# Performance work log

Measured on AMD Instinct MI355X. Metric: run time of the kernel, lower is better.

The kernel has to match this reference:

```python
import jax, jax.numpy as jnp
import numpy as np

N, M, D = 100000, 5000, 2

def setup_inputs() -> dict:
    key = jax.random.key(0)
    k1, k2, k3 = jax.random.split(key, 3)
    euclidean_data = jax.random.normal(k1, (N, D), dtype=jnp.float32)
    maze_points = jax.random.normal(k2, (M, D), dtype=jnp.float32)
    ts_proj = jax.random.uniform(k3, (M,), dtype=jnp.float32)
    return {"euclidean_data": euclidean_data, "maze_points": maze_points, "ts_proj": ts_proj}

def reference(euclidean_data, maze_points, ts_proj):
    # squared distance matrix [N, M], reduced via argmin (1-NN)
    diff = euclidean_data[:, None, :] - maze_points[None, :, :]   # [N, M, D]
    dist2 = jnp.sum(jnp.square(diff), axis=-1)                    # [N, M]
    best = jnp.argmin(dist2, axis=1)                              # [N]
    projected_pos = maze_points[best]                             # [N, D]
    linear_pos = ts_proj[best]                                    # [N]
    return (projected_pos, linear_pos)
```

## Files before the change

kernel.cpp:

```cpp
#include <hip/hip_runtime.h>

#define N_Q  100000
#define N_M  5000
#define G    64
#define NC   (G * G)
#define RMAX 4
#define CS_OFF_B   64
#define SORT_OFF_B (CS_OFF_B + 16400)
#define OVF_OFF_B  (SORT_OFF_B + N_M * 16)
#define WS_NEED    (OVF_OFF_B + N_Q * 4)

__global__ __launch_bounds__(1024) void build_grid(
    const float* __restrict__ maze, const float* __restrict__ ts,
    float* __restrict__ ws)
{
    __shared__ float red[1024];
    __shared__ int   part[1024];
    __shared__ int   cnt[NC];
    const int t = threadIdx.x;
    if (t == 0) ((int*)ws)[8] = 0;

    float mnx = 1e30f, mxx = -1e30f, mny = 1e30f, mxy = -1e30f;
    for (int i = t; i < N_M; i += 1024) {
        const float x = maze[2 * i], y = maze[2 * i + 1];
        mnx = fminf(mnx, x); mxx = fmaxf(mxx, x);
        mny = fminf(mny, y); mxy = fmaxf(mxy, y);
    }
    auto reduce = [&](float v, bool domin) -> float {
        red[t] = v; __syncthreads();
        for (int s = 512; s > 0; s >>= 1) {
            if (t < s) {
                const float o = red[t + s];
                red[t] = domin ? fminf(red[t], o) : fmaxf(red[t], o);
            }
            __syncthreads();
        }
        const float r = red[0]; __syncthreads(); return r;
    };
    mnx = reduce(mnx, true);  mxx = reduce(mxx, false);
    mny = reduce(mny, true);  mxy = reduce(mxy, false);

    float cwx = (mxx - mnx) * (1.0f / G) * (1.0f + 1e-5f);
    float cwy = (mxy - mny) * (1.0f / G) * (1.0f + 1e-5f);
    if (!(cwx > 0.0f)) cwx = 1.0f;
    if (!(cwy > 0.0f)) cwy = 1.0f;
    const float ivx = 1.0f / cwx, ivy = 1.0f / cwy;
    if (t == 0) {
        ws[0] = mnx; ws[1] = mny; ws[2] = cwx;
        ws[3] = cwy; ws[4] = ivx; ws[5] = ivy;
    }

    for (int i = t; i < NC; i += 1024) cnt[i] = 0;
    __syncthreads();
    for (int i = t; i < N_M; i += 1024) {
        const float x = maze[2 * i], y = maze[2 * i + 1];
        const int cx = min(G - 1, max(0, (int)((x - mnx) * ivx)));
        const int cy = min(G - 1, max(0, (int)((y - mny) * ivy)));
        atomicAdd(&cnt[cy * G + cx], 1);
    }
    __syncthreads();

    int* cs = (int*)((char*)ws + CS_OFF_B);
    const int base = t * 4;
    int loc[4], sum = 0;
    #pragma unroll
    for (int j = 0; j < 4; ++j) { loc[j] = sum; sum += cnt[base + j]; }
    part[t] = sum; __syncthreads();
    for (int s = 1; s < 1024; s <<= 1) {
        const int v = (t >= s) ? part[t - s] : 0;
        __syncthreads();
        part[t] += v;
        __syncthreads();
    }
    const int excl = part[t] - sum;
    #pragma unroll
    for (int j = 0; j < 4; ++j) cs[base + j] = excl + loc[j];
    if (t == 0) cs[NC] = N_M;
    __syncthreads();
    #pragma unroll
    for (int j = 0; j < 4; ++j) cnt[base + j] = excl + loc[j];
    __syncthreads();

    float4* sorted = (float4*)((char*)ws + SORT_OFF_B);
    for (int i = t; i < N_M; i += 1024) {
        const float x = maze[2 * i], y = maze[2 * i + 1];
        const int cx = min(G - 1, max(0, (int)((x - mnx) * ivx)));
        const int cy = min(G - 1, max(0, (int)((y - mny) * ivy)));
        const int pos = atomicAdd(&cnt[cy * G + cx], 1);
        float4 e; e.x = x; e.y = y; e.z = ts[i]; e.w = __int_as_float(i);
        sorted[pos] = e;
    }
}

__global__ __launch_bounds__(256) void grid_query(
    const float* __restrict__ q, const float* __restrict__ maze,
    const float* __restrict__ ts, float* __restrict__ ws,
    float* __restrict__ out)
{
    const int qi = blockIdx.x * 256 + threadIdx.x;
    if (qi >= N_Q) return;

    const float mnx = ws[0], mny = ws[1], cwx = ws[2];
    const float cwy = ws[3], ivx = ws[4], ivy = ws[5];
    const int*    cs     = (const int*)((const char*)ws + CS_OFF_B);
    const float4* sorted = (const float4*)((const char*)ws + SORT_OFF_B);

    const float2 Q = ((const float2*)q)[qi];
    const float qx = Q.x, qy = Q.y;
    const int cx = min(G - 1, max(0, (int)((qx - mnx) * ivx)));
    const int cy = min(G - 1, max(0, (int)((qy - mny) * ivy)));

    float bd2 = 3.4e38f;
    int bidx = 0x7fffffff;

    auto cand = [&](const float4 c) {
        const float dx = __fsub_rn(qx, c.x);
        const float dy = __fsub_rn(qy, c.y);
        const float d2 = __fadd_rn(__fmul_rn(dx, dx), __fmul_rn(dy, dy));
        const int idx = __float_as_int(c.w);
        if (d2 < bd2 || (d2 == bd2 && idx < bidx)) { bd2 = d2; bidx = idx; }
    };
    auto scan8 = [&](int s, int e) {
        for (int p = s; p < e; p += 8) {
            const float4 c0 = sorted[p];
            const float4 c1 = sorted[p + 1 < e ? p + 1 : p];
            const float4 c2 = sorted[p + 2 < e ? p + 2 : p];
            const float4 c3 = sorted[p + 3 < e ? p + 3 : p];
            const float4 c4 = sorted[p + 4 < e ? p + 4 : p];
            const float4 c5 = sorted[p + 5 < e ? p + 5 : p];
            const float4 c6 = sorted[p + 6 < e ? p + 6 : p];
            const float4 c7 = sorted[p + 7 < e ? p + 7 : p];
            cand(c0); cand(c1); cand(c2); cand(c3);
            cand(c4); cand(c5); cand(c6); cand(c7);
        }
    };
    auto scan4 = [&](int s, int e) {
        for (int p = s; p < e; p += 4) {
            const float4 c0 = sorted[p];
            const float4 c1 = sorted[p + 1 < e ? p + 1 : p];
            const float4 c2 = sorted[p + 2 < e ? p + 2 : p];
            const float4 c3 = sorted[p + 3 < e ? p + 3 : p];
            cand(c0); cand(c1); cand(c2); cand(c3);
        }
    };
    auto bound_ok = [&](int r) -> bool {
        const float Xlo = mnx + (float)(cx - r) * cwx;
        const float Xhi = mnx + (float)(cx + r + 1) * cwx;
        const float Ylo = mny + (float)(cy - r) * cwy;
        const float Yhi = mny + (float)(cy + r + 1) * cwy;
        float lb = fminf(fminf(qx - Xlo, Xhi - qx), fminf(qy - Ylo, Yhi - qy));
        lb = lb * 0.9999f - 1e-6f;
        return (lb > 0.0f) && (lb * lb > bd2);
    };

    {
        const int x0 = max(0, cx - 1), x1 = min(G - 1, cx + 1);
        const int rA = max(0, cy - 1) * G, rB = cy * G, rC = min(G - 1, cy + 1) * G;
        const int sA = cs[rA + x0], eA = cs[rA + x1 + 1];
        const int sB = cs[rB + x0], eB = cs[rB + x1 + 1];
        const int sC = cs[rC + x0], eC = cs[rC + x1 + 1];
        scan8(sA, eA); scan8(sB, eB); scan8(sC, eC);
    }
    bool resolved = bound_ok(1);

    for (int r = 2; r <= RMAX && __any(!resolved); ++r) {
        if (!resolved) {
            const int X0 = max(0, cx - r), X1 = min(G - 1, cx + r);
            if (cy - r >= 0)     { const int rb = (cy - r) * G; scan8(cs[rb + X0], cs[rb + X1 + 1]); }
            if (cy + r <= G - 1) { const int rb = (cy + r) * G; scan8(cs[rb + X0], cs[rb + X1 + 1]); }
            const int Y0 = max(0, cy - r + 1), Y1 = min(G - 1, cy + r - 1);
            if (cx - r >= 0)     for (int y = Y0; y <= Y1; ++y) { const int c0 = y * G + cx - r; scan4(cs[c0], cs[c0 + 1]); }
            if (cx + r <= G - 1) for (int y = Y0; y <= Y1; ++y) { const int c0 = y * G + cx + r; scan4(cs[c0], cs[c0 + 1]); }
            resolved = bound_ok(r);
        }
    }

    if (resolved) {
        out[2 * qi]       = maze[2 * bidx];
        out[2 * qi + 1]   = maze[2 * bidx + 1];
        out[2 * N_Q + qi] = ts[bidx];
    } else {
        int* ovfc = (int*)ws + 8;
        const int pos = atomicAdd(ovfc, 1);
        ((int*)((char*)ws + OVF_OFF_B))[pos] = qi;
    }
}

__global__ __launch_bounds__(256) void brute_overflow(
    const float* __restrict__ q, const float* __restrict__ maze,
    const float* __restrict__ ts, const float* __restrict__ ws,
    float* __restrict__ out)
{
    const int cnt = ((const int*)ws)[8];
    const int* ovl = (const int*)((const char*)ws + OVF_OFF_B);
    const int wave  = (blockIdx.x * 256 + threadIdx.x) >> 6;
    const int lane  = threadIdx.x & 63;
    const int nwave = gridDim.x * 4;

    for (int w = wave; w < cnt; w += nwave) {
        const int qi = ovl[w];
        const float qx = q[2 * qi], qy = q[2 * qi + 1];
        float bd2 = 3.4e38f; int bidx = 0x7fffffff;
        for (int p = lane; p < N_M; p += 64) {
            const float2 c = ((const float2*)maze)[p];
            const float dx = __fsub_rn(qx, c.x);
            const float dy = __fsub_rn(qy, c.y);
            const float d2 = __fadd_rn(__fmul_rn(dx, dx), __fmul_rn(dy, dy));
            if (d2 < bd2 || (d2 == bd2 && p < bidx)) { bd2 = d2; bidx = p; }
        }
        #pragma unroll
        for (int s = 1; s < 64; s <<= 1) {
            const float ob = __shfl_xor(bd2, s);
            const int   oi = __shfl_xor(bidx, s);
            if (ob < bd2 || (ob == bd2 && oi < bidx)) { bd2 = ob; bidx = oi; }
        }
        if (lane == 0) {
            out[2 * qi]       = maze[2 * bidx];
            out[2 * qi + 1]   = maze[2 * bidx + 1];
            out[2 * N_Q + qi] = ts[bidx];
        }
    }
}

#define CW   4
#define CHK  1264
#define NPAD (CW * CHK)

typedef float v2f __attribute__((ext_vector_type(2)));
typedef float v8f __attribute__((ext_vector_type(8)));

__global__ void setup_soa(const float* __restrict__ maze, float* __restrict__ ws) {
    const int i = blockIdx.x * 256 + threadIdx.x;
    if (i >= NPAD) return;
    const int c = i / CHK, k = i - c * CHK;
    float x = 1e30f, y = 1e30f;
    const int g = c * 1250 + k;
    if (k < 1250) { x = -maze[2 * g]; y = -maze[2 * g + 1]; }
    ws[i] = x;
    ws[NPAD + i] = y;
}

#define LDX0(D) asm volatile("s_load_dwordx8 %0, %1, 0x0"    : "=s"(D) : "s"(xb))
#define LDX1(D) asm volatile("s_load_dwordx8 %0, %1, 0x20"   : "=s"(D) : "s"(xb))
#define LDY0(D) asm volatile("s_load_dwordx8 %0, %1, 0x4f00" : "=s"(D) : "s"(xb))
#define LDY1(D) asm volatile("s_load_dwordx8 %0, %1, 0x4f20" : "=s"(D) : "s"(xb))
#define WAIT4(a,b,c,d) asm volatile("s_waitcnt lgkmcnt(0)" : "+s"(a), "+s"(b), "+s"(c), "+s"(d))

#define PSTEP(X8, Y8, J) do {                                                 \
    v2f px_ = __builtin_shufflevector(X8, X8, 2*(J), 2*(J)+1);                \
    v2f py_ = __builtin_shufflevector(Y8, Y8, 2*(J), 2*(J)+1);                \
    v2f dx_, dy_;                                                             \
    asm("v_pk_add_f32 %0, %1, %2" : "=v"(dx_) : "s"(px_), "v"(qxx));          \
    asm("v_pk_add_f32 %0, %1, %2" : "=v"(dy_) : "s"(py_), "v"(qyy));          \
    asm("v_pk_mul_f32 %0, %0, %0" : "+v"(dx_));                               \
    asm("v_pk_mul_f32 %0, %0, %0" : "+v"(dy_));                               \
    asm("v_pk_add_f32 %0, %0, %1" : "+v"(dx_) : "v"(dy_));                    \
    float a_ = dx_.x, b_ = dx_.y;                                             \
    asm("v_min3_f32 %0, %1, %2, %0" : "+v"(bm) : "v"(a_), "v"(b_));           \
} while (0)

#define COMP(X0, X1, Y0, Y1, B) do {                                          \
    PSTEP(X0, Y0, 0); PSTEP(X0, Y0, 1); PSTEP(X0, Y0, 2); PSTEP(X0, Y0, 3);   \
    PSTEP(X1, Y1, 0); PSTEP(X1, Y1, 1); PSTEP(X1, Y1, 2); PSTEP(X1, Y1, 3);   \
    bb = (bm < prev) ? (B) : bb; prev = bm;                                   \
} while (0)

__global__ __launch_bounds__(256) void nn_scan(
    const float* __restrict__ q, const float* __restrict__ maze,
    const float* __restrict__ ts, const float* __restrict__ ws,
    float* __restrict__ out)
{
    __shared__ float sval[CW][64];
    __shared__ int   sidx[CW][64];
    const int lane = threadIdx.x & 63;
    const int wv   = __builtin_amdgcn_readfirstlane((int)(threadIdx.x >> 6));
    const int qi   = blockIdx.x * 64 + lane;
    const int qc   = qi < N_Q ? qi : N_Q - 1;
    const float2 Q = ((const float2*)q)[qc];
    const v2f qxx = { Q.x, Q.x };
    const v2f qyy = { Q.y, Q.y };
    unsigned long long xb = (unsigned long long)(const void*)(ws + (size_t)wv * CHK);
    v8f ax0, ax1, ay0, ay1, bx0, bx1, by0, by1;
    LDX0(ax0); LDX1(ax1); LDY0(ay0); LDY1(ay1); xb += 64;
    float bm = 3.4e38f, prev = 3.4e38f;
    int bb = 0;
    #pragma unroll 1
    for (int k = 0; k < 39; ++k) {
        WAIT4(ax0, ax1, ay0, ay1);
        LDX0(bx0); LDX1(bx1); LDY0(by0); LDY1(by1); xb += 64;
        COMP(ax0, ax1, ay0, ay1, 2 * k);
        WAIT4(bx0, bx1, by0, by1);
        LDX0(ax0); LDX1(ax1); LDY0(ay0); LDY1(ay1); xb += 64;
        COMP(bx0, bx1, by0, by1, 2 * k + 1);
    }
    WAIT4(ax0, ax1, ay0, ay1);
    COMP(ax0, ax1, ay0, ay1, 78);
    int fk = 0x7fffffff;
    {
        const float* xs = ws + (size_t)wv * CHK + (size_t)bb * 16;
        #pragma unroll
        for (int j = 0; j < 16; ++j) {
            const float dx = __fadd_rn(Q.x, xs[j]);
            const float dy = __fadd_rn(Q.y, xs[j + NPAD]);
            const float d2 = __fadd_rn(__fmul_rn(dx, dx), __fmul_rn(dy, dy));
            if (d2 == bm) fk = min(fk, bb * 16 + j);
        }
    }
    const int kloc = fk < 1250 ? fk : 1249;
    sval[wv][lane] = bm;
    sidx[wv][lane] = wv * 1250 + kloc;
    __syncthreads();
    if (wv == 0 && qi < N_Q) {
        float bv = sval[0][lane];
        int   bg = sidx[0][lane];
        #pragma unroll
        for (int c = 1; c < CW; ++c) {
            const float v = sval[c][lane];
            const int   g = sidx[c][lane];
            if (v < bv || (v == bv && g < bg)) { bv = v; bg = g; }
        }
        const float2 bp = ((const float2*)maze)[bg];
        out[2 * qi]       = bp.x;
        out[2 * qi + 1]   = bp.y;
        out[2 * N_Q + qi] = ts[bg];
    }
}

extern "C" void kernel_launch(void* const* d_in, const int* in_sizes, int n_in,
                              void* d_out, int out_size, void* d_ws, size_t ws_size,
                              hipStream_t stream) {
    const float* q    = (const float*)d_in[0];
    const float* maze = (const float*)d_in[1];
    const float* ts   = (const float*)d_in[2];
    float* out = (float*)d_out;

    if (ws_size >= (size_t)WS_NEED) {
        build_grid<<<1, 1024, 0, stream>>>(maze, ts, (float*)d_ws);
        grid_query<<<(N_Q + 255) / 256, 256, 0, stream>>>(q, maze, ts,
                                                          (float*)d_ws, out);
        brute_overflow<<<256, 256, 0, stream>>>(q, maze, ts, (const float*)d_ws, out);
    } else {
        setup_soa<<<(NPAD + 255) / 256, 256, 0, stream>>>(maze, (float*)d_ws);
        nn_scan<<<(N_Q + 63) / 64, 256, 0, stream>>>(q, maze, ts,
                                                     (const float*)d_ws, out);
    }
}
```

Measured before the change: 73.65 us.

## Stage grid into LDS per block and use wave-shuffle reductions in grid build

Measured after the change: 87.06 us. 18.2% more time.

```diff
diff --git a/kernel.cpp b/kernel.cpp
--- a/kernel.cpp
+++ b/kernel.cpp
@@ -14,10 +14,10 @@
     const float* __restrict__ maze, const float* __restrict__ ts,
     float* __restrict__ ws)
 {
-    __shared__ float red[1024];
-    __shared__ int   part[1024];
     __shared__ int   cnt[NC];
-    const int t = threadIdx.x;
+    __shared__ float wred[16][4];
+    __shared__ int   wsum[16];
+    const int t = threadIdx.x, lane = t & 63, wv = t >> 6;
     if (t == 0) ((int*)ws)[8] = 0;
 
     float mnx = 1e30f, mxx = -1e30f, mny = 1e30f, mxy = -1e30f;
@@ -26,32 +26,28 @@
         mnx = fminf(mnx, x); mxx = fmaxf(mxx, x);
         mny = fminf(mny, y); mxy = fmaxf(mxy, y);
     }
-    auto reduce = [&](float v, bool domin) -> float {
-        red[t] = v; __syncthreads();
-        for (int s = 512; s > 0; s >>= 1) {
-            if (t < s) {
-                const float o = red[t + s];
-                red[t] = domin ? fminf(red[t], o) : fmaxf(red[t], o);
-            }
-            __syncthreads();
-        }
-        const float r = red[0]; __syncthreads(); return r;
-    };
-    mnx = reduce(mnx, true);  mxx = reduce(mxx, false);
-    mny = reduce(mny, true);  mxy = reduce(mxy, false);
-
+    #pragma unroll
+    for (int s = 1; s < 64; s <<= 1) {
+        mnx = fminf(mnx, __shfl_xor(mnx, s));
+        mxx = fmaxf(mxx, __shfl_xor(mxx, s));
+        mny = fminf(mny, __shfl_xor(mny, s));
+        mxy = fmaxf(mxy, __shfl_xor(mxy, s));
+    }
+    if (lane == 0) { wred[wv][0] = mnx; wred[wv][1] = mxx; wred[wv][2] = mny; wred[wv][3] = mxy; }
+    for (int i = t; i < NC; i += 1024) cnt[i] = 0;
+    __syncthreads();
+    #pragma unroll
+    for (int w = 0; w < 16; ++w) {
+        mnx = fminf(mnx, wred[w][0]); mxx = fmaxf(mxx, wred[w][1]);
+        mny = fminf(mny, wred[w][2]); mxy = fmaxf(mxy, wred[w][3]);
+    }
     float cwx = (mxx - mnx) * (1.0f / G) * (1.0f + 1e-5f);
     float cwy = (mxy - mny) * (1.0f / G) * (1.0f + 1e-5f);
     if (!(cwx > 0.0f)) cwx = 1.0f;
     if (!(cwy > 0.0f)) cwy = 1.0f;
     const float ivx = 1.0f / cwx, ivy = 1.0f / cwy;
-    if (t == 0) {
-        ws[0] = mnx; ws[1] = mny; ws[2] = cwx;
-        ws[3] = cwy; ws[4] = ivx; ws[5] = ivy;
-    }
-
-    for (int i = t; i < NC; i += 1024) cnt[i] = 0;
-    __syncthreads();
+    if (t == 0) { ws[0] = mnx; ws[1] = mny; ws[2] = cwx; ws[3] = cwy; ws[4] = ivx; ws[5] = ivy; }
+
     for (int i = t; i < N_M; i += 1024) {
         const float x = maze[2 * i], y = maze[2 * i + 1];
         const int cx = min(G - 1, max(0, (int)((x - mnx) * ivx)));
@@ -65,18 +61,20 @@
     int loc[4], sum = 0;
     #pragma unroll
     for (int j = 0; j < 4; ++j) { loc[j] = sum; sum += cnt[base + j]; }
-    part[t] = sum; __syncthreads();
-    for (int s = 1; s < 1024; s <<= 1) {
-        const int v = (t >= s) ? part[t - s] : 0;
-        __syncthreads();
-        part[t] += v;
-        __syncthreads();
-    }
-    const int excl = part[t] - sum;
+    int incl = sum;
+    #pragma unroll
+    for (int s = 1; s < 64; s <<= 1) {
+        const int o = __shfl_up(incl, s);
+        if (lane >= s) incl += o;
+    }
+    if (lane == 63) wsum[wv] = incl;
+    __syncthreads();
+    int wbase = 0;
+    for (int w = 0; w < 16; ++w) wbase += (w < wv) ? wsum[w] : 0;
+    const int excl = wbase + incl - sum;
     #pragma unroll
     for (int j = 0; j < 4; ++j) cs[base + j] = excl + loc[j];
     if (t == 0) cs[NC] = N_M;
-    __syncthreads();
     #pragma unroll
     for (int j = 0; j < 4; ++j) cnt[base + j] = excl + loc[j];
     __syncthreads();
@@ -97,18 +95,23 @@
     const float* __restrict__ ts, float* __restrict__ ws,
     float* __restrict__ out)
 {
+    __shared__ int    lcs[NC + 1];
+    __shared__ float4 lpt[N_M];
+
+    const int*    gcs = (const int*)((const char*)ws + CS_OFF_B);
+    const float4* gpt = (const float4*)((const char*)ws + SORT_OFF_B);
+    for (int i = threadIdx.x; i < NC + 1; i += 256) lcs[i] = gcs[i];
+    for (int i = threadIdx.x; i < N_M; i += 256)    lpt[i] = gpt[i];
+
     const int qi = blockIdx.x * 256 + threadIdx.x;
-    if (qi >= N_Q) return;
-
+    const int qc = qi < N_Q ? qi : N_Q - 1;
     const float mnx = ws[0], mny = ws[1], cwx = ws[2];
     const float cwy = ws[3], ivx = ws[4], ivy = ws[5];
-    const int*    cs     = (const int*)((const char*)ws + CS_OFF_B);
-    const float4* sorted = (const float4*)((const char*)ws + SORT_OFF_B);
-
-    const float2 Q = ((const float2*)q)[qi];
+    const float2 Q = ((const float2*)q)[qc];
     const float qx = Q.x, qy = Q.y;
     const int cx = min(G - 1, max(0, (int)((qx - mnx) * ivx)));
     const int cy = min(G - 1, max(0, (int)((qy - mny) * ivy)));
+    __syncthreads();
 
     float bd2 = 3.4e38f;
     int bidx = 0x7fffffff;
@@ -122,25 +125,16 @@
     };
     auto scan8 = [&](int s, int e) {
         for (int p = s; p < e; p += 8) {
-            const float4 c0 = sorted[p];
-            const float4 c1 = sorted[p + 1 < e ? p + 1 : p];
-            const float4 c2 = sorted[p + 2 < e ? p + 2 : p];
-            const float4 c3 = sorted[p + 3 < e ? p + 3 : p];
-            const float4 c4 = sorted[p + 4 < e ? p + 4 : p];
-            const float4 c5 = sorted[p + 5 < e ? p + 5 : p];
-            const float4 c6 = sorted[p + 6 < e ? p + 6 : p];
-            const float4 c7 = sorted[p + 7 < e ? p + 7 : p];
+            const float4 c0 = lpt[p];
+            const float4 c1 = lpt[p + 1 < e ? p + 1 : p];
+            const float4 c2 = lpt[p + 2 < e ? p + 2 : p];
+            const float4 c3 = lpt[p + 3 < e ? p + 3 : p];
+            const float4 c4 = lpt[p + 4 < e ? p + 4 : p];
+            const float4 c5 = lpt[p + 5 < e ? p + 5 : p];
+            const float4 c6 = lpt[p + 6 < e ? p + 6 : p];
+            const float4 c7 = lpt[p + 7 < e ? p + 7 : p];
             cand(c0); cand(c1); cand(c2); cand(c3);
             cand(c4); cand(c5); cand(c6); cand(c7);
-        }
-    };
-    auto scan4 = [&](int s, int e) {
-        for (int p = s; p < e; p += 4) {
-            const float4 c0 = sorted[p];
-            const float4 c1 = sorted[p + 1 < e ? p + 1 : p];
-            const float4 c2 = sorted[p + 2 < e ? p + 2 : p];
-            const float4 c3 = sorted[p + 3 < e ? p + 3 : p];
-            cand(c0); cand(c1); cand(c2); cand(c3);
         }
     };
     auto bound_ok = [&](int r) -> bool {
@@ -156,33 +150,34 @@
     {
         const int x0 = max(0, cx - 1), x1 = min(G - 1, cx + 1);
         const int rA = max(0, cy - 1) * G, rB = cy * G, rC = min(G - 1, cy + 1) * G;
-        const int sA = cs[rA + x0], eA = cs[rA + x1 + 1];
-        const int sB = cs[rB + x0], eB = cs[rB + x1 + 1];
-        const int sC = cs[rC + x0], eC = cs[rC + x1 + 1];
-        scan8(sA, eA); scan8(sB, eB); scan8(sC, eC);
+        scan8(lcs[rA + x0], lcs[rA + x1 + 1]);
+        scan8(lcs[rB + x0], lcs[rB + x1 + 1]);
+        scan8(lcs[rC + x0], lcs[rC + x1 + 1]);
     }
     bool resolved = bound_ok(1);
 
     for (int r = 2; r <= RMAX && __any(!resolved); ++r) {
         if (!resolved) {
             const int X0 = max(0, cx - r), X1 = min(G - 1, cx + r);
-            if (cy - r >= 0)     { const int rb = (cy - r) * G; scan8(cs[rb + X0], cs[rb + X1 + 1]); }
-            if (cy + r <= G - 1) { const int rb = (cy + r) * G; scan8(cs[rb + X0], cs[rb + X1 + 1]); }
+            if (cy - r >= 0)     { const int rb = (cy - r) * G; scan8(lcs[rb + X0], lcs[rb + X1 + 1]); }
+            if (cy + r <= G - 1) { const int rb = (cy + r) * G; scan8(lcs[rb + X0], lcs[rb + X1 + 1]); }
             const int Y0 = max(0, cy - r + 1), Y1 = min(G - 1, cy + r - 1);
-            if (cx - r >= 0)     for (int y = Y0; y <= Y1; ++y) { const int c0 = y * G + cx - r; scan4(cs[c0], cs[c0 + 1]); }
-            if (cx + r <= G - 1) for (int y = Y0; y <= Y1; ++y) { const int c0 = y * G + cx + r; scan4(cs[c0], cs[c0 + 1]); }
+            if (cx - r >= 0)     for (int y = Y0; y <= Y1; ++y) { const int c0 = y * G + cx - r; scan8(lcs[c0], lcs[c0 + 1]); }
+            if (cx + r <= G - 1) for (int y = Y0; y <= Y1; ++y) { const int c0 = y * G + cx + r; scan8(lcs[c0], lcs[c0 + 1]); }
             resolved = bound_ok(r);
         }
     }
 
-    if (resolved) {
-        out[2 * qi]       = maze[2 * bidx];
-        out[2 * qi + 1]   = maze[2 * bidx + 1];
-        out[2 * N_Q + qi] = ts[bidx];
-    } else {
-        int* ovfc = (int*)ws + 8;
-        const int pos = atomicAdd(ovfc, 1);
-        ((int*)((char*)ws + OVF_OFF_B))[pos] = qi;
+    if (qi < N_Q) {
+        if (resolved) {
+            out[2 * qi]       = maze[2 * bidx];
+            out[2 * qi + 1]   = maze[2 * bidx + 1];
+            out[2 * N_Q + qi] = ts[bidx];
+        } else {
+            int* ovfc = (int*)ws + 8;
+            const int pos = atomicAdd(ovfc, 1);
+            ((int*)((char*)ws + OVF_OFF_B))[pos] = qi;
+        }
     }
 }
 
@@ -338,7 +333,7 @@
         build_grid<<<1, 1024, 0, stream>>>(maze, ts, (float*)d_ws);
         grid_query<<<(N_Q + 255) / 256, 256, 0, stream>>>(q, maze, ts,
                                                           (float*)d_ws, out);
-        brute_overflow<<<256, 256, 0, stream>>>(q, maze, ts, (const float*)d_ws, out);
+        brute_overflow<<<128, 256, 0, stream>>>(q, maze, ts, (const float*)d_ws, out);
     } else {
         setup_soa<<<(NPAD + 255) / 256, 256, 0, stream>>>(maze, (float*)d_ws);
         nn_scan<<<(N_Q + 63) / 64, 256, 0, stream>>>(q, maze, ts,
```

## Parallelize grid build, sort queries by cell, use finer fixed-bounds grid

Applied to the files above, without the earlier changes.

After: 111.2 us. +50.9%, slower.

```diff
diff --git a/kernel.cpp b/kernel.cpp
--- a/kernel.cpp
+++ b/kernel.cpp
@@ -2,117 +2,122 @@
 
 #define N_Q  100000
 #define N_M  5000
-#define G    64
+#define G    128
 #define NC   (G * G)
-#define RMAX 4
-#define CS_OFF_B   64
-#define SORT_OFF_B (CS_OFF_B + 16400)
-#define OVF_OFF_B  (SORT_OFF_B + N_M * 16)
-#define WS_NEED    (OVF_OFF_B + N_Q * 4)
-
-__global__ __launch_bounds__(1024) void build_grid(
-    const float* __restrict__ maze, const float* __restrict__ ts,
+#define RMAX 6
+#define MNX  (-6.0f)
+#define MNY  (-6.0f)
+#define CWC  0.09375f
+#define IVC  (1.0f / CWC)
+
+#define MC_OFF_B   64
+#define QC_OFF_B   (MC_OFF_B + NC * 4)
+#define SORT_OFF_B (QC_OFF_B + NC * 4)
+#define SQ_OFF_B   (SORT_OFF_B + N_M * 16)
+#define OVF_OFF_B  (SQ_OFF_B + N_Q * 4)
+#define OVF_CAP    32768
+#define WS_NEED    (OVF_OFF_B + OVF_CAP * 4)
+#define ZERO_INTS  ((MC_OFF_B + 2 * NC * 4) / 4)
+
+__device__ __forceinline__ int cell_of(float x, float y) {
+    int cx = (int)((x - MNX) * IVC);
+    int cy = (int)((y - MNY) * IVC);
+    cx = min(G - 1, max(0, cx));
+    cy = min(G - 1, max(0, cy));
+    return cy * G + cx;
+}
+
+__global__ void k_zero(int* ws) {
+    const int i = blockIdx.x * 256 + threadIdx.x;
+    for (int j = i; j < ZERO_INTS; j += gridDim.x * 256) ws[j] = 0;
+}
+
+__global__ __launch_bounds__(256) void k_hist(
+    const float* __restrict__ q, const float* __restrict__ maze,
     float* __restrict__ ws)
 {
-    __shared__ float red[1024];
-    __shared__ int   part[1024];
-    __shared__ int   cnt[NC];
-    const int t = threadIdx.x;
-    if (t == 0) ((int*)ws)[8] = 0;
-
-    float mnx = 1e30f, mxx = -1e30f, mny = 1e30f, mxy = -1e30f;
-    for (int i = t; i < N_M; i += 1024) {
-        const float x = maze[2 * i], y = maze[2 * i + 1];
-        mnx = fminf(mnx, x); mxx = fmaxf(mxx, x);
-        mny = fminf(mny, y); mxy = fmaxf(mxy, y);
-    }
-    auto reduce = [&](float v, bool domin) -> float {
-        red[t] = v; __syncthreads();
-        for (int s = 512; s > 0; s >>= 1) {
-            if (t < s) {
-                const float o = red[t + s];
-                red[t] = domin ? fminf(red[t], o) : fmaxf(red[t], o);
-            }
-            __syncthreads();
-        }
-        const float r = red[0]; __syncthreads(); return r;
-    };
-    mnx = reduce(mnx, true);  mxx = reduce(mxx, false);
-    mny = reduce(mny, true);  mxy = reduce(mxy, false);
-
-    float cwx = (mxx - mnx) * (1.0f / G) * (1.0f + 1e-5f);
-    float cwy = (mxy - mny) * (1.0f / G) * (1.0f + 1e-5f);
-    if (!(cwx > 0.0f)) cwx = 1.0f;
-    if (!(cwy > 0.0f)) cwy = 1.0f;
-    const float ivx = 1.0f / cwx, ivy = 1.0f / cwy;
-    if (t == 0) {
-        ws[0] = mnx; ws[1] = mny; ws[2] = cwx;
-        ws[3] = cwy; ws[4] = ivx; ws[5] = ivy;
-    }
-
-    for (int i = t; i < NC; i += 1024) cnt[i] = 0;
-    __syncthreads();
-    for (int i = t; i < N_M; i += 1024) {
-        const float x = maze[2 * i], y = maze[2 * i + 1];
-        const int cx = min(G - 1, max(0, (int)((x - mnx) * ivx)));
-        const int cy = min(G - 1, max(0, (int)((y - mny) * ivy)));
-        atomicAdd(&cnt[cy * G + cx], 1);
-    }
-    __syncthreads();
-
-    int* cs = (int*)((char*)ws + CS_OFF_B);
-    const int base = t * 4;
-    int loc[4], sum = 0;
-    #pragma unroll
-    for (int j = 0; j < 4; ++j) { loc[j] = sum; sum += cnt[base + j]; }
-    part[t] = sum; __syncthreads();
-    for (int s = 1; s < 1024; s <<= 1) {
-        const int v = (t >= s) ? part[t - s] : 0;
+    const int i = blockIdx.x * 256 + threadIdx.x;
+    int* mc = (int*)((char*)ws + MC_OFF_B);
+    int* qc = (int*)((char*)ws + QC_OFF_B);
+    if (i < N_M) {
+        const float2 p = ((const float2*)maze)[i];
+        atomicAdd(&mc[cell_of(p.x, p.y)], 1);
+    }
+    if (i < N_Q) {
+        const float2 p = ((const float2*)q)[i];
+        atomicAdd(&qc[cell_of(p.x, p.y)], 1);
+    }
+}
+
+__global__ __launch_bounds__(1024) void k_scan(float* __restrict__ ws) {
+    __shared__ int wsum[16];
+    const int t = threadIdx.x, lane = t & 63, wv = t >> 6;
+    int* arr0 = (int*)((char*)ws + MC_OFF_B);
+    int* arr1 = (int*)((char*)ws + QC_OFF_B);
+    for (int a = 0; a < 2; ++a) {
+        int* arr = a ? arr1 : arr0;
+        const int base = t * 16;
+        int loc[16], sum = 0;
+        #pragma unroll
+        for (int j = 0; j < 16; ++j) { loc[j] = sum; sum += arr[base + j]; }
+        int incl = sum;
+        #pragma unroll
+        for (int s = 1; s < 64; s <<= 1) {
+            const int o = __shfl_up(incl, s);
+            if (lane >= s) incl += o;
+        }
+        if (lane == 63) wsum[wv] = incl;
         __syncthreads();
-        part[t] += v;
+        int wbase = 0;
+        #pragma unroll
+        for (int w = 0; w < 16; ++w) wbase += (w < wv) ? wsum[w] : 0;
+        const int excl = wbase + incl - sum;
+        #pragma unroll
+        for (int j = 0; j < 16; ++j) arr[base + j] = excl + loc[j];
         __syncthreads();
     }
-    const int excl = part[t] - sum;
-    #pragma unroll
-    for (int j = 0; j < 4; ++j) cs[base + j] = excl + loc[j];
-    if (t == 0) cs[NC] = N_M;
-    __syncthreads();
-    #pragma unroll
-    for (int j = 0; j < 4; ++j) cnt[base + j] = excl + loc[j];
-    __syncthreads();
-
-    float4* sorted = (float4*)((char*)ws + SORT_OFF_B);
-    for (int i = t; i < N_M; i += 1024) {
-        const float x = maze[2 * i], y = maze[2 * i + 1];
-        const int cx = min(G - 1, max(0, (int)((x - mnx) * ivx)));
-        const int cy = min(G - 1, max(0, (int)((y - mny) * ivy)));
-        const int pos = atomicAdd(&cnt[cy * G + cx], 1);
-        float4 e; e.x = x; e.y = y; e.z = ts[i]; e.w = __int_as_float(i);
-        sorted[pos] = e;
+}
+
+__global__ __launch_bounds__(256) void k_scat(
+    const float* __restrict__ q, const float* __restrict__ maze,
+    const float* __restrict__ ts, float* __restrict__ ws)
+{
+    const int i = blockIdx.x * 256 + threadIdx.x;
+    int* mc = (int*)((char*)ws + MC_OFF_B);
+    int* qc = (int*)((char*)ws + QC_OFF_B);
+    if (i < N_M) {
+        const float2 p = ((const float2*)maze)[i];
+        const int pos = atomicAdd(&mc[cell_of(p.x, p.y)], 1);
+        float4 e; e.x = p.x; e.y = p.y; e.z = ts[i]; e.w = __int_as_float(i);
+        ((float4*)((char*)ws + SORT_OFF_B))[pos] = e;
+    }
+    if (i < N_Q) {
+        const float2 p = ((const float2*)q)[i];
+        const int pos = atomicAdd(&qc[cell_of(p.x, p.y)], 1);
+        ((int*)((char*)ws + SQ_OFF_B))[pos] = i;
     }
 }
 
 __global__ __launch_bounds__(256) void grid_query(
-    const float* __restrict__ q, const float* __restrict__ maze,
-    const float* __restrict__ ts, float* __restrict__ ws,
+    const float* __restrict__ q, float* __restrict__ ws,
     float* __restrict__ out)
 {
-    const int qi = blockIdx.x * 256 + threadIdx.x;
-    if (qi >= N_Q) return;
-
-    const float mnx = ws[0], mny = ws[1], cwx = ws[2];
-    const float cwy = ws[3], ivx = ws[4], ivy = ws[5];
-    const int*    cs     = (const int*)((const char*)ws + CS_OFF_B);
+    const int ii = blockIdx.x * 256 + threadIdx.x;
+    const int si = ii < N_Q ? ii : N_Q - 1;
+    const int qi = ((const int*)((const char*)ws + SQ_OFF_B))[si];
+
+    const int*    mc     = (const int*)((const char*)ws + MC_OFF_B);
     const float4* sorted = (const float4*)((const char*)ws + SORT_OFF_B);
 
     const float2 Q = ((const float2*)q)[qi];
     const float qx = Q.x, qy = Q.y;
-    const int cx = min(G - 1, max(0, (int)((qx - mnx) * ivx)));
-    const int cy = min(G - 1, max(0, (int)((qy - mny) * ivy)));
+    int cx = (int)((qx - MNX) * IVC); cx = min(G - 1, max(0, cx));
+    int cy = (int)((qy - MNY) * IVC); cy = min(G - 1, max(0, cy));
 
     float bd2 = 3.4e38f;
     int bidx = 0x7fffffff;
 
+    auto cstart = [&](int c) -> int { return c ? mc[c - 1] : 0; };
     auto cand = [&](const float4 c) {
         const float dx = __fsub_rn(qx, c.x);
         const float dy = __fsub_rn(qy, c.y);
@@ -134,20 +139,127 @@
             cand(c4); cand(c5); cand(c6); cand(c7);
         }
     };
-    auto scan4 = [&](int s, int e) {
-        for (int p = s; p < e; p += 4) {
+    auto bound_ok = [&](int r) -> bool {
+        const float Xlo = MNX + (float)(cx - r) * CWC;
+        const float Xhi = MNX + (float)(cx + r + 1) * CWC;
+        const float Ylo = MNY + (float)(cy - r) * CWC;
+        const float Yhi = MNY + (float)(cy + r + 1) * CWC;
+        float lb = fminf(fminf(qx - Xlo, Xhi - qx), fminf(qy - Ylo, Yhi - qy));
+        lb = lb * 0.9999f - 1e-6f;
+        return (lb > 0.0f) && (lb * lb > bd2);
+    };
+
+    {
+        const int x0 = max(0, cx - 1), x1 = min(G - 1, cx + 1);
+        const int rA = max(0, cy - 1) * G, rB = cy * G, rC = min(G - 1, cy + 1) * G;
+        scan8(cstart(rA + x0), mc[rA + x1]);
+        scan8(cstart(rB + x0), mc[rB + x1]);
+        scan8(cstart(rC + x0), mc[rC + x1]);
+    }
+    bool resolved = bound_ok(1);
+
+    for (int r = 2; r <= RMAX && __any(!resolved); ++r) {
+        if (!resolved) {
+            const int X0 = max(0, cx - r), X1 = min(G - 1, cx + r);
+            if (cy - r >= 0)     { const int rb = (cy - r) * G; scan8(cstart(rb + X0), mc[rb + X1]); }
+            if (cy + r <= G - 1) { const int rb = (cy + r) * G; scan8(cstart(rb + X0), mc[rb + X1]); }
+            const int Y0 = max(0, cy - r + 1), Y1 = min(G - 1, cy + r - 1);
+            if (cx - r >= 0)     for (int y = Y0; y <= Y1; ++y) { const int c0 = y * G + cx - r; scan8(cstart(c0), mc[c0]); }
+            if (cx + r <= G - 1) for (int y = Y0; y <= Y1; ++y) { const int c0 = y * G + cx + r; scan8(cstart(c0), mc[c0]); }
+            resolved = bound_ok(r);
+        }
+    }
+
+    if (ii < N_Q) {
+        if (resolved) {
+            const float2 bp = ((const float2*)((const char*)ws + SORT_OFF_B))[0];
+            (void)bp;
+            out[2 * qi]       = q[0] * 0.0f + ((const float*)0, 0.0f);
+        }
+    }
+    if (ii < N_Q) {
+        if (resolved) {
+            const float* mazeF = (const float*)nullptr;
+            (void)mazeF;
+        }
+    }
+    if (ii < N_Q) {
+        if (resolved) {
+            const float2* mzp = (const float2*)((const char*)ws + 0); (void)mzp;
+        }
+    }
+    if (ii < N_Q) {
+        int* ovfc = (int*)ws;
+        if (!resolved) {
+            const int pos = atomicAdd(ovfc, 1);
+            if (pos < OVF_CAP) {
+                ((int*)((char*)ws + OVF_OFF_B))[pos] = qi;
+            } else {
+                float vb = 3.4e38f; int vi = 0x7fffffff;
+                for (int p = 0; p < N_M; ++p) {
+                    const float4 c = sorted[p];
+                    const float dx = __fsub_rn(qx, c.x);
+                    const float dy = __fsub_rn(qy, c.y);
+                    const float d2 = __fadd_rn(__fmul_rn(dx, dx), __fmul_rn(dy, dy));
+                    const int idx = __float_as_int(c.w);
+                    if (d2 < vb || (d2 == vb && idx < vi)) { vb = d2; vi = idx; }
+                }
+                bd2 = vb; bidx = vi; resolved = true;
+            }
+        }
+        if (resolved) {
+            out[2 * N_Q + qi] = 0.0f;
+        }
+    }
+}
+
+__global__ __launch_bounds__(256) void grid_query2(
+    const float* __restrict__ q, const float* __restrict__ maze,
+    const float* __restrict__ ts, float* __restrict__ ws,
+    float* __restrict__ out)
+{
+    const int ii = blockIdx.x * 256 + threadIdx.x;
+    const int si = ii < N_Q ? ii : N_Q - 1;
+    const int qi = ((const int*)((const char*)ws + SQ_OFF_B))[si];
+
+    const int*    mc     = (const int*)((const char*)ws + MC_OFF_B);
+    const float4* sorted = (const float4*)((const char*)ws + SORT_OFF_B);
+
+    const float2 Q = ((const float2*)q)[qi];
+    const float qx = Q.x, qy = Q.y;
+    int cx = (int)((qx - MNX) * IVC); cx = min(G - 1, max(0, cx));
+    int cy = (int)((qy - MNY) * IVC); cy = min(G - 1, max(0, cy));
+
+    float bd2 = 3.4e38f;
+    int bidx = 0x7fffffff;
+
+    auto cstart = [&](int c) -> int { return c ? mc[c - 1] : 0; };
+    auto cand = [&](const float4 c) {
+        const float dx = __fsub_rn(qx, c.x);
+        const float dy = __fsub_rn(qy, c.y);
+        const float d2 = __fadd_rn(__fmul_rn(dx, dx), __fmul_rn(dy, dy));
+        const int idx = __float_as_int(c.w);
+        if (d2 < bd2 || (d2 == bd2 && idx < bidx)) { bd2 = d2; bidx = idx; }
+    };
+    auto scan8 = [&](int s, int e) {
+        for (int p = s; p < e; p += 8) {
             const float4 c0 = sorted[p];
             const float4 c1 = sorted[p + 1 < e ? p + 1 : p];
             const float4 c2 = sorted[p + 2 < e ? p + 2 : p];
             const float4 c3 = sorted[p + 3 < e ? p + 3 : p];
+            const float4 c4 = sorted[p + 4 < e ? p + 4 : p];
+            const float4 c5 = sorted[p + 5 < e ? p + 5 : p];
+            const float4 c6 = sorted[p + 6 < e ? p + 6 : p];
+            const float4 c7 = sorted[p + 7 < e ? p + 7 : p];
             cand(c0); cand(c1); cand(c2); cand(c3);
+            cand(c4); cand(c5); cand(c6); cand(c7);
         }
     };
     auto bound_ok = [&](int r) -> bool {
-        const float Xlo = mnx + (float)(cx - r) * cwx;
-        const float Xhi = mnx + (float)(cx + r + 1) * cwx;
-        const float Ylo = mny + (float)(cy - r) * cwy;
-        const float Yhi = mny + (float)(cy + r + 1) * cwy;
+        const float Xlo = MNX + (float)(cx - r) * CWC;
+        const float Xhi = MNX + (float)(cx + r + 1) * CWC;
+        const float Ylo = MNY + (float)(cy - r) * CWC;
+        const float Yhi = MNY + (float)(cy + r + 1) * CWC;
         float lb = fminf(fminf(qx - Xlo, Xhi - qx), fminf(qy - Ylo, Yhi - qy));
         lb = lb * 0.9999f - 1e-6f;
         return (lb > 0.0f) && (lb * lb > bd2);
@@ -156,33 +268,47 @@
     {
         const int x0 = max(0, cx - 1), x1 = min(G - 1, cx + 1);
         const int rA = max(0, cy - 1) * G, rB = cy * G, rC = min(G - 1, cy + 1) * G;
-        const int sA = cs[rA + x0], eA = cs[rA + x1 + 1];
-        const int sB = cs[rB + x0], eB = cs[rB + x1 + 1];
-        const int sC = cs[rC + x0], eC = cs[rC + x1 + 1];
-        scan8(sA, eA); scan8(sB, eB); scan8(sC, eC);
+        scan8(cstart(rA + x0), mc[rA + x1]);
+        scan8(cstart(rB + x0), mc[rB + x1]);
+        scan8(cstart(rC + x0), mc[rC + x1]);
     }
     bool resolved = bound_ok(1);
 
     for (int r = 2; r <= RMAX && __any(!resolved); ++r) {
         if (!resolved) {
             const int X0 = max(0, cx - r), X1 = min(G - 1, cx + r);
-            if (cy - r >= 0)     { const int rb = (cy - r) * G; scan8(cs[rb + X0], cs[rb + X1 + 1]); }
-            if (cy + r <= G - 1) { const int rb = (cy + r) * G; scan8(cs[rb + X0], cs[rb + X1 + 1]); }
+            if (cy - r >= 0)     { const int rb = (cy - r) * G; scan8(cstart(rb + X0), mc[rb + X1]); }
+            if (cy + r <= G - 1) { const int rb = (cy + r) * G; scan8(cstart(rb + X0), mc[rb + X1]); }
             const int Y0 = max(0, cy - r + 1), Y1 = min(G - 1, cy + r - 1);
-            if (cx - r >= 0)     for (int y = Y0; y <= Y1; ++y) { const int c0 = y * G + cx - r; scan4(cs[c0], cs[c0 + 1]); }
-            if (cx + r <= G - 1) for (int y = Y0; y <= Y1; ++y) { const int c0 = y * G + cx + r; scan4(cs[c0], cs[c0 + 1]); }
+            if (cx - r >= 0)     for (int y = Y0; y <= Y1; ++y) { const int c0 = y * G + cx - r; scan8(cstart(c0), mc[c0]); }
+            if (cx + r <= G - 1) for (int y = Y0; y <= Y1; ++y) { const int c0 = y * G + cx + r; scan8(cstart(c0), mc[c0]); }
             resolved = bound_ok(r);
         }
     }
 
-    if (resolved) {
-        out[2 * qi]       = maze[2 * bidx];
-        out[2 * qi + 1]   = maze[2 * bidx + 1];
-        out[2 * N_Q + qi] = ts[bidx];
-    } else {
-        int* ovfc = (int*)ws + 8;
-        const int pos = atomicAdd(ovfc, 1);
-        ((int*)((char*)ws + OVF_OFF_B))[pos] = qi;
+    if (ii < N_Q) {
+        if (resolved) {
+            out[2 * qi]       = maze[2 * bidx];
+            out[2 * qi + 1]   = maze[2 * bidx + 1];
+            out[2 * N_Q + qi] = ts[bidx];
+        } else {
+            const int pos = atomicAdd((int*)ws, 1);
+            if (pos < OVF_CAP) {
+                ((int*)((char*)ws + OVF_OFF_B))[pos] = qi;
+            } else {
+                float vb = 3.4e38f; int vi = 0x7fffffff;
+                for (int p = 0; p < N_M; ++p) {
+                    const float2 c = ((const float2*)maze)[p];
+                    const float dx = __fsub_rn(qx, c.x);
+                    const float dy = __fsub_rn(qy, c.y);
+                    const float d2 = __fadd_rn(__fmul_rn(dx, dx), __fmul_rn(dy, dy));
+                    if (d2 < vb || (d2 == vb && p < vi)) { vb = d2; vi = p; }
+                }
+                out[2 * qi]       = maze[2 * vi];
+                out[2 * qi + 1]   = maze[2 * vi + 1];
+                out[2 * N_Q + qi] = ts[vi];
+            }
+        }
     }
 }
 
@@ -191,7 +317,8 @@
     const float* __restrict__ ts, const float* __restrict__ ws,
     float* __restrict__ out)
 {
-    const int cnt = ((const int*)ws)[8];
+    int cnt = ((const int*)ws)[0];
+    cnt = cnt < OVF_CAP ? cnt : OVF_CAP;
     const int* ovl = (const int*)((const char*)ws + OVF_OFF_B);
     const int wave  = (blockIdx.x * 256 + threadIdx.x) >> 6;
     const int lane  = threadIdx.x & 63;
@@ -222,9 +349,9 @@
     }
 }
 
-#define CW   4
+#define CW_   4
 #define CHK  1264
-#define NPAD (CW * CHK)
+#define NPAD (CW_ * CHK)
 
 typedef float v2f __attribute__((ext_vector_type(2)));
 typedef float v8f __attribute__((ext_vector_type(8)));
@@ -270,8 +397,8 @@
     const float* __restrict__ ts, const float* __restrict__ ws,
     float* __restrict__ out)
 {
-    __shared__ float sval[CW][64];
-    __shared__ int   sidx[CW][64];
+    __shared__ float sval[CW_][64];
+    __shared__ int   sidx[CW_][64];
     const int lane = threadIdx.x & 63;
     const int wv   = __builtin_amdgcn_readfirstlane((int)(threadIdx.x >> 6));
     const int qi   = blockIdx.x * 64 + lane;
@@ -314,7 +441,7 @@
         float bv = sval[0][lane];
         int   bg = sidx[0][lane];
         #pragma unroll
-        for (int c = 1; c < CW; ++c) {
+        for (int c = 1; c < CW_; ++c) {
             const float v = sval[c][lane];
             const int   g = sidx[c][lane];
             if (v < bv || (v == bv && g < bg)) { bv = v; bg = g; }
@@ -335,10 +462,13 @@
     float* out = (float*)d_out;
 
     if (ws_size >= (size_t)WS_NEED) {
-        build_grid<<<1, 1024, 0, stream>>>(maze, ts, (float*)d_ws);
-        grid_query<<<(N_Q + 255) / 256, 256, 0, stream>>>(q, maze, ts,
-                                                          (float*)d_ws, out);
-        brute_overflow<<<256, 256, 0, stream>>>(q, maze, ts, (const float*)d_ws, out);
+        float* ws = (float*)d_ws;
+        k_zero<<<64, 256, 0, stream>>>((int*)d_ws);
+        k_hist<<<(N_Q + 255) / 256, 256, 0, stream>>>(q, maze, ws);
+        k_scan<<<1, 1024, 0, stream>>>(ws);
+        k_scat<<<(N_Q + 255) / 256, 256, 0, stream>>>(q, maze, ts, ws);
+        grid_query2<<<(N_Q + 255) / 256, 256, 0, stream>>>(q, maze, ts, ws, out);
+        brute_overflow<<<128, 256, 0, stream>>>(q, maze, ts, (const float*)ws, out);
     } else {
         setup_soa<<<(NPAD + 255) / 256, 256, 0, stream>>>(maze, (float*)d_ws);
         nn_scan<<<(N_Q + 63) / 64, 256, 0, stream>>>(q, maze, ts,
```
